# Performance work log

Measured on AMD Instinct MI355X. Metric: run time of the kernel, lower is better.

The kernel has to match this reference:

```python
import jax, jax.numpy as jnp
import numpy as np

N = 20000      # total nodes (1000 graphs x 20 nodes)
E = 160000     # total edges (avg degree 8)
B = 1000       # number of graphs
H = 2          # attention heads
C = 128        # out_channels per head (encoder_hidden)
D = H * C      # 256, node feature dim between layers
EMB = 64       # embed_dim / LSTM hidden
V = 5          # vocab
T = 21         # max_length decode steps
SOS = 1        # NT2IDX['U']
SQRT_C = float(np.sqrt(C))


def setup_inputs() -> dict:
    key = jax.random.key(0)
    ks = jax.random.split(key, 40)
    rn = lambda k, shape, s=0.05: (jax.random.normal(k, shape) * s).astype(jnp.float32)
    p = {}
    p['x'] = jax.random.normal(ks[0], (N, 4), jnp.float32)
    p['edge_index'] = jax.random.randint(ks[1], (2, E), 0, N)
    p['batch'] = jnp.repeat(jnp.arange(B), N // B)  # contiguous graph ids, all graphs nonempty
    p['gc_content'] = jax.random.uniform(ks[2], (B,), jnp.float32)
    p['seq_length'] = jnp.full((B,), 21.0, jnp.float32)
    # layer 0 TransformerConv (in=4 -> heads*C=256)
    p['c0_wq'] = rn(ks[3], (4, D)); p['c0_bq'] = rn(ks[4], (D,))
    p['c0_wk'] = rn(ks[5], (4, D)); p['c0_bk'] = rn(ks[6], (D,))
    p['c0_wv'] = rn(ks[7], (4, D)); p['c0_bv'] = rn(ks[8], (D,))
    p['c0_ws'] = rn(ks[9], (4, D)); p['c0_bs'] = rn(ks[10], (D,))
    # layers 1..2 stacked (in=256 -> 256)
    p['cw_q'] = rn(ks[11], (2, D, D)); p['cb_q'] = rn(ks[12], (2, D))
    p['cw_k'] = rn(ks[13], (2, D, D)); p['cb_k'] = rn(ks[14], (2, D))
    p['cw_v'] = rn(ks[15], (2, D, D)); p['cb_v'] = rn(ks[16], (2, D))
    p['cw_s'] = rn(ks[17], (2, D, D)); p['cb_s'] = rn(ks[18], (2, D))
    p['ln_g'] = jnp.ones((3, D), jnp.float32)
    p['ln_b'] = jnp.zeros((3, D), jnp.float32)
    p['enc_w'] = rn(ks[19], (D + 2, EMB)); p['enc_b'] = rn(ks[20], (EMB,))
    p['emb'] = rn(ks[21], (V, EMB), 1.0)
    p['w_ih'] = rn(ks[22], (EMB, 4 * EMB)); p['w_hh'] = rn(ks[23], (EMB, 4 * EMB))
    p['b_ih'] = rn(ks[24], (4 * EMB,)); p['b_hh'] = rn(ks[25], (4 * EMB,))
    p['fc_w'] = rn(ks[26], (EMB, V)); p['fc_b'] = rn(ks[27], (V,))
    return p


def _transformer_conv(x, src, tgt, wq, bq, wk, bk, wv, bv, ws, bs):
    # PyG TransformerConv, heads=H, concat=True, root_weight=True, no edge_attr.
    n = x.shape[0]
    q = (x @ wq + bq).reshape(n, H, C)[tgt]   # [E,H,C] query at target nodes
    k = (x @ wk + bk).reshape(n, H, C)[src]   # [E,H,C] key at source nodes
    v = (x @ wv + bv).reshape(n, H, C)[src]   # [E,H,C] value at source nodes
    score = (q * k).sum(-1) / SQRT_C          # [E,H]
    m = jax.ops.segment_max(score, tgt, num_segments=n)   # scatter-softmax (stable)
    a = jnp.exp(score - m[tgt])
    den = jax.ops.segment_sum(a, tgt, num_segments=n)
    alpha = a / den[tgt]                      # [E,H]
    out = jax.ops.segment_sum(alpha[..., None] * v, tgt, num_segments=n)  # [N,H,C]
    return out.reshape(n, D) + x @ ws + bs    # concat heads + skip (lin_skip)


def _layer_norm(x, g, b):
    mu = x.mean(-1, keepdims=True)
    var = ((x - mu) ** 2).mean(-1, keepdims=True)
    return (x - mu) * jax.lax.rsqrt(var + 1e-5) * g + b


def reference(x, edge_index, batch, gc_content, seq_length,
              c0_wq, c0_bq, c0_wk, c0_bk, c0_wv, c0_bv, c0_ws, c0_bs,
              cw_q, cb_q, cw_k, cb_k, cw_v, cb_v, cw_s, cb_s,
              ln_g, ln_b, enc_w, enc_b, emb, w_ih, w_hh, b_ih, b_hh, fc_w, fc_b):
    src, tgt = edge_index[0], edge_index[1]
    # ---- encoder: 3 TransformerConv + ReLU + LayerNorm (dropout=eval/identity) ----
    h = _transformer_conv(x, src, tgt, c0_wq, c0_bq, c0_wk, c0_bk, c0_wv, c0_bv, c0_ws, c0_bs)
    h = _layer_norm(jax.nn.relu(h), ln_g[0], ln_b[0])
    for i in range(2):
        h = _transformer_conv(h, src, tgt, cw_q[i], cb_q[i], cw_k[i], cb_k[i],
                              cw_v[i], cb_v[i], cw_s[i], cb_s[i])
        h = _layer_norm(jax.nn.relu(h), ln_g[i + 1], ln_b[i + 1])
    # ---- global mean pool per graph ----
    counts = jax.ops.segment_sum(jnp.ones((h.shape[0],), h.dtype), batch, num_segments=B)
    pool = jax.ops.segment_sum(h, batch, num_segments=B) / jnp.maximum(counts, 1.0)[:, None]
    gfeat = jnp.concatenate([pool, gc_content[:, None], seq_length[:, None]], axis=1)  # [B,258]
    enc = jax.nn.relu(gfeat @ enc_w + enc_b)  # [B,EMB]
    def step(carry, _):
        hs, cs, inp = carry
        g = inp @ w_ih + b_ih + hs @ w_hh + b_hh      # [B,4*EMB], torch gate order i,f,g,o
        i_g, f_g, g_g, o_g = jnp.split(g, 4, axis=-1)
        cs = jax.nn.sigmoid(f_g) * cs + jax.nn.sigmoid(i_g) * jnp.tanh(g_g)
        hs = jax.nn.sigmoid(o_g) * jnp.tanh(cs)
        logits = hs @ fc_w + fc_b                     # [B,V]
        tok = jnp.argmax(logits, axis=-1)
        return (hs, cs, emb[tok]), logits
    init = (enc, jnp.zeros_like(enc), jnp.broadcast_to(emb[SOS], (B, EMB)))
    _, logits = jax.lax.scan(step, init, None, length=T)  # [T,B,V]
    return jnp.transpose(logits, (1, 0, 2))               # [B,T,V]
```

## Files before the change

### kernel.cpp

```cpp
#include <hip/hip_runtime.h>
#include <math.h>

#define NN 20000
#define NNP 20096
#define NE 160000
#define NB 1000
#define EMB 64
#define NV 5
#define NT 21

typedef __attribute__((ext_vector_type(8))) short bf16x8;
typedef __attribute__((ext_vector_type(4))) float f32x4;

__device__ __forceinline__ float sigm(float x) { return 1.f / (1.f + expf(-x)); }

__device__ __forceinline__ ushort f2bf(float x) {
    unsigned u = __float_as_uint(x);
    unsigned r = (u + 0x7FFFu + ((u >> 16) & 1u)) >> 16;
    return (ushort)r;
}
__device__ __forceinline__ float bf2f(ushort h) {
    return __uint_as_float(((unsigned)h) << 16);
}

__device__ __forceinline__ void gl16(const ushort* g, ushort* l) {
    __builtin_amdgcn_global_load_lds((const __attribute__((address_space(1))) void*)g,
                                     (__attribute__((address_space(3))) void*)l, 16, 0, 0);
}

__global__ void k_fill(unsigned* p, int n, unsigned v) {
    int i = blockIdx.x * 256 + threadIdx.x;
    if (i < n) p[i] = v;
}

__global__ void k_count(const int* __restrict__ ei, int* __restrict__ deg,
                        int* __restrict__ bucket) {
    int e = blockIdx.x * 256 + threadIdx.x;
    if (e >= NE) return;
    int s = ei[e], t = ei[NE + e];
    int pos = atomicAdd(&deg[t], 1);
    if (pos < 64) bucket[(size_t)t * 64 + pos] = s;
}

__global__ void k_lin0(const float* __restrict__ x,
                       const float* __restrict__ wq, const float* __restrict__ bq,
                       const float* __restrict__ wk, const float* __restrict__ bk,
                       const float* __restrict__ wv, const float* __restrict__ bv,
                       const float* __restrict__ wss, const float* __restrict__ bss,
                       float* __restrict__ qkv, float* __restrict__ acc) {
    int idx = blockIdx.x * 256 + threadIdx.x;
    if (idx >= NN * 1024) return;
    int n = idx >> 10, j = idx & 1023;
    float x0 = x[n*4+0], x1 = x[n*4+1], x2 = x[n*4+2], x3 = x[n*4+3];
    const float* W; const float* bb; int col; float* outp;
    if (j < 256)      { W = wq;  bb = bq;  col = j;       outp = qkv + (size_t)n*768 + j; }
    else if (j < 512) { W = wk;  bb = bk;  col = j - 256; outp = qkv + (size_t)n*768 + j; }
    else if (j < 768) { W = wv;  bb = bv;  col = j - 512; outp = qkv + (size_t)n*768 + j; }
    else              { W = wss; bb = bss; col = j - 768; outp = acc + (size_t)n*256 + col; }
    float v = bb[col] + x0*W[col] + x1*W[256+col] + x2*W[512+col] + x3*W[768+col];
    *outp = v;
}

__global__ void k_convW(const float* __restrict__ cwq, const float* __restrict__ cwk,
                        const float* __restrict__ cwv, const float* __restrict__ cws,
                        ushort* __restrict__ WtHT, ushort* __restrict__ WtLT) {
    int idx = blockIdx.x * 256 + threadIdx.x;
    if (idx >= 2 * 64 * 1024) return;
    int n = idx & 1023;
    int rest = idx >> 10;
    int kq = rest & 63;
    int l = rest >> 6;
    int wsel = n >> 8, col = n & 255;
    const float* W = (wsel == 0) ? cwq : (wsel == 1) ? cwk : (wsel == 2) ? cwv : cws;
    W += (size_t)l * 65536;
    ushort hv[4], lv[4];
    #pragma unroll
    for (int i = 0; i < 4; ++i) {
        float v = W[(size_t)(kq * 4 + i) * 256 + col];
        hv[i] = f2bf(v);
        lv[i] = f2bf(v - bf2f(hv[i]));
    }
    int k0 = kq * 4;
    int kt = k0 >> 5, c = (k0 >> 3) & 3, j0 = k0 & 7;
    size_t o = ((size_t)l * 32 * 1024 + (size_t)(kt * 4 + c) * 1024 + n) * 8 + j0;
    *(ushort4*)(WtHT + o) = make_ushort4(hv[0], hv[1], hv[2], hv[3]);
    *(ushort4*)(WtLT + o) = make_ushort4(lv[0], lv[1], lv[2], lv[3]);
}

__global__ __launch_bounds__(256) void k_gemm4_mfma(
    const ushort* __restrict__ AhT, const ushort* __restrict__ AlT,
    const ushort* __restrict__ WtHT, const ushort* __restrict__ WtLT,
    const float* __restrict__ bq, const float* __restrict__ bk,
    const float* __restrict__ bv, const float* __restrict__ bs,
    float* __restrict__ qkv, float* __restrict__ acc) {
    __shared__ __align__(16) ushort SMEM[2][4][4][128][8];

    int id = blockIdx.x;
    int xcd = id & 7;
    int q8 = id >> 3;
    int s8 = q8 >> 3;
    int cblk = q8 & 7;
    int rblk = xcd + 8 * s8;
    if (rblk >= 157) return;
    int row0 = rblk * 128;
    int wsel = cblk >> 1;
    int coll = (cblk & 1) * 128;
    const float* bias; float* C; int ldc;
    if (wsel == 0)      { bias = bq; C = qkv;       ldc = 768; }
    else if (wsel == 1) { bias = bk; C = qkv + 256; ldc = 768; }
    else if (wsel == 2) { bias = bv; C = qkv + 512; ldc = 768; }
    else                { bias = bs; C = acc;       ldc = 256; }
    int ncol0 = cblk * 128;

    int tid = threadIdx.x;
    int w = tid >> 6, lane = tid & 63;
    int wr = w >> 1, wc = w & 1;
    int g = lane >> 4, r16 = lane & 15;

    const ushort* srcp; int rbase, rstr;
    if (w == 0)      { srcp = AhT;  rbase = row0;  rstr = NNP; }
    else if (w == 1) { srcp = AlT;  rbase = row0;  rstr = NNP; }
    else if (w == 2) { srcp = WtHT; rbase = ncol0; rstr = 1024; }
    else             { srcp = WtLT; rbase = ncol0; rstr = 1024; }
    ushort* lb0 = &SMEM[0][w][0][0][0];
    ushort* lb1 = &SMEM[1][w][0][0][0];

    const ushort* ap[8];
    #pragma unroll
    for (int i = 0; i < 8; ++i)
        ap[i] = srcp + ((size_t)((i >> 1) * rstr + rbase + (i & 1) * 64 + lane)) * 8;
    const size_t kstep = (size_t)4 * rstr * 8;

    f32x4 accv[4][4];
    f32x4 zz = {0.f, 0.f, 0.f, 0.f};
    #pragma unroll
    for (int m = 0; m < 4; ++m)
        #pragma unroll
        for (int n = 0; n < 4; ++n) accv[m][n] = zz;

    auto stage = [&](ushort* lb) {
        #pragma unroll
        for (int i = 0; i < 8; ++i) {
            gl16(ap[i], lb + i * 512);
            ap[i] += kstep;
        }
    };

    stage(lb0);
    for (int kt = 0; kt < 8; ++kt) {
        int cur = kt & 1;
        if (kt < 7) {
            stage(cur ? lb0 : lb1);
            asm volatile("s_waitcnt vmcnt(8)" ::: "memory");
        } else {
            asm volatile("s_waitcnt vmcnt(0)" ::: "memory");
        }
        __builtin_amdgcn_sched_barrier(0);
        __builtin_amdgcn_s_barrier();

        bf16x8 bH[4], bL[4];
        #pragma unroll
        for (int n = 0; n < 4; ++n) {
            int rw = wc * 64 + n * 16 + r16;
            bH[n] = *(const bf16x8*)&SMEM[cur][2][g][rw][0];
            bL[n] = *(const bf16x8*)&SMEM[cur][3][g][rw][0];
        }
        #pragma unroll
        for (int m = 0; m < 4; ++m) {
            int rw = wr * 64 + m * 16 + r16;
            bf16x8 aH = *(const bf16x8*)&SMEM[cur][0][g][rw][0];
            bf16x8 aL = *(const bf16x8*)&SMEM[cur][1][g][rw][0];
            #pragma unroll
            for (int n = 0; n < 4; ++n) {
                accv[m][n] = __builtin_amdgcn_mfma_f32_16x16x32_bf16(aH, bH[n], accv[m][n], 0, 0, 0);
                accv[m][n] = __builtin_amdgcn_mfma_f32_16x16x32_bf16(aH, bL[n], accv[m][n], 0, 0, 0);
                accv[m][n] = __builtin_amdgcn_mfma_f32_16x16x32_bf16(aL, bH[n], accv[m][n], 0, 0, 0);
            }
        }
        __builtin_amdgcn_s_barrier();
    }

    float* sl = (float*)&SMEM[0][0][0][0][0] + w * 1088;
    int erow = lane >> 2;
    int ecb  = (lane & 3) * 16;
    #pragma unroll
    for (int m = 0; m < 4; ++m) {
        #pragma unroll
        for (int n = 0; n < 4; ++n) {
            int cl = coll + wc * 64 + n * 16 + r16;
            float bvv = bias[cl];
            #pragma unroll
            for (int r = 0; r < 4; ++r)
                sl[(g * 4 + r) * 68 + n * 16 + r16] = accv[m][n][r] + bvv;
        }
        int grow = row0 + wr * 64 + m * 16 + erow;
        if (grow < NN) {
            float4 v0 = *(float4*)&sl[erow * 68 + ecb + 0];
            float4 v1 = *(float4*)&sl[erow * 68 + ecb + 4];
            float4 v2 = *(float4*)&sl[erow * 68 + ecb + 8];
            float4 v3 = *(float4*)&sl[erow * 68 + ecb + 12];
            float* cp = C + (size_t)grow * ldc + coll + wc * 64 + ecb;
            ((float4*)cp)[0] = v0; ((float4*)cp)[1] = v1;
            ((float4*)cp)[2] = v2; ((float4*)cp)[3] = v3;
        }
    }
}

__global__ __launch_bounds__(256) void k_attn_ln(const float* __restrict__ qkv,
                                                 const int* __restrict__ deg,
                                                 const int* __restrict__ bucket,
                                                 const float* __restrict__ acc,
                                                 const float* __restrict__ lg,
                                                 const float* __restrict__ lb,
                                                 ushort* __restrict__ AhT,
                                                 ushort* __restrict__ AlT) {
    __shared__ float ssc[4][64];
    __shared__ int ssrc[4][64];
    __shared__ __align__(16) float srow[2][256];
    int ws = threadIdx.x >> 6, l = threadIdx.x & 63;
    int t = blockIdx.x * 2 + (ws >> 1);
    int h = ws & 1;
    int cnt = deg[t]; if (cnt > 64) cnt = 64;
    const int* bptr = bucket + (size_t)t * 64;
    int gq = l >> 4, pos = l & 15;
    const float* qp = qkv + (size_t)t * 768 + h * 128 + pos * 8;
    float4 qa = *(const float4*)qp, qb = *(const float4*)(qp + 4);

    float m = -INFINITY, den = 0.f, o0 = 0.f, o1 = 0.f;
    for (int c0 = 0; c0 < cnt; c0 += 64) {
        int clen = cnt - c0; if (clen > 64) clen = 64;
        if (l < clen) ssrc[ws][l] = bptr[c0 + l];
        for (int e = gq; e < clen; e += 4) {
            int s = ssrc[ws][e];
            const float* kp = qkv + (size_t)s * 768 + 256 + h * 128 + pos * 8;
            float4 ka = *(const float4*)kp, kb = *(const float4*)(kp + 4);
            float d = qa.x*ka.x + qa.y*ka.y + qa.z*ka.z + qa.w*ka.w
                    + qb.x*kb.x + qb.y*kb.y + qb.z*kb.z + qb.w*kb.w;
            d += __shfl_xor(d, 1); d += __shfl_xor(d, 2);
            d += __shfl_xor(d, 4); d += __shfl_xor(d, 8);
            if (pos == 0) ssc[ws][e] = d * 0.08838834764831845f;
        }
        float sv = (l < clen) ? ssc[ws][l] : -INFINITY;
        float M = sv;
        #pragma unroll
        for (int off = 32; off; off >>= 1) M = fmaxf(M, __shfl_xor(M, off));
        float wl = (l < clen) ? expf(sv - M) : 0.f;
        float D = wl;
        #pragma unroll
        for (int off = 32; off; off >>= 1) D += __shfl_xor(D, off);
        ssc[ws][l] = wl;
        float nm = fmaxf(m, M);
        float so = expf(m - nm), sn = expf(M - nm);
        den = den * so + D * sn;
        o0 *= so; o1 *= so;
        float co0 = 0.f, co1 = 0.f;
        int p = 0;
        for (; p + 4 <= clen; p += 4) {
            float a0 = ssc[ws][p],     a1 = ssc[ws][p + 1];
            float a2 = ssc[ws][p + 2], a3 = ssc[ws][p + 3];
            int s0 = ssrc[ws][p],     s1 = ssrc[ws][p + 1];
            int s2 = ssrc[ws][p + 2], s3 = ssrc[ws][p + 3];
            float2 v0 = *(const float2*)(qkv + (size_t)s0 * 768 + 512 + h * 128 + l * 2);
            float2 v1 = *(const float2*)(qkv + (size_t)s1 * 768 + 512 + h * 128 + l * 2);
            float2 v2 = *(const float2*)(qkv + (size_t)s2 * 768 + 512 + h * 128 + l * 2);
            float2 v3 = *(const float2*)(qkv + (size_t)s3 * 768 + 512 + h * 128 + l * 2);
            co0 += a0 * v0.x + a1 * v1.x + a2 * v2.x + a3 * v3.x;
            co1 += a0 * v0.y + a1 * v1.y + a2 * v2.y + a3 * v3.y;
        }
        for (; p < clen; ++p) {
            float a = ssc[ws][p];
            int s = ssrc[ws][p];
            float2 v = *(const float2*)(qkv + (size_t)s * 768 + 512 + h * 128 + l * 2);
            co0 += a * v.x; co1 += a * v.y;
        }
        o0 += co0 * sn; o1 += co1 * sn;
        m = nm;
    }
    float inv = (den > 0.f) ? 1.f / den : 0.f;
    float2 sk = *(const float2*)(acc + (size_t)t * 256 + h * 128 + l * 2);
    float v0 = fmaxf(sk.x + o0 * inv, 0.f);
    float v1 = fmaxf(sk.y + o1 * inv, 0.f);
    *(float2*)&srow[ws >> 1][h * 128 + l * 2] = make_float2(v0, v1);
    __syncthreads();
    if (ws < 2) {
        int tt = blockIdx.x * 2 + ws;
        float4 v = *(const float4*)&srow[ws][l * 4];
        float sum = v.x + v.y + v.z + v.w;
        #pragma unroll
        for (int o = 32; o; o >>= 1) sum += __shfl_xor(sum, o);
        float mu = sum * (1.f / 256.f);
        float d0 = v.x - mu, d1 = v.y - mu, d2 = v.z - mu, d3 = v.w - mu;
        float sq = d0*d0 + d1*d1 + d2*d2 + d3*d3;
        #pragma unroll
        for (int o = 32; o; o >>= 1) sq += __shfl_xor(sq, o);
        float rs = rsqrtf(sq * (1.f / 256.f) + 1e-5f);
        int d = l * 4;
        float4 gg = *(const float4*)(lg + d);
        float4 bb = *(const float4*)(lb + d);
        float e0 = d0 * rs * gg.x + bb.x;
        float e1 = d1 * rs * gg.y + bb.y;
        float e2 = d2 * rs * gg.z + bb.z;
        float e3 = d3 * rs * gg.w + bb.w;
        ushort4 hv, lv;
        hv.x = f2bf(e0); lv.x = f2bf(e0 - bf2f(hv.x));
        hv.y = f2bf(e1); lv.y = f2bf(e1 - bf2f(hv.y));
        hv.z = f2bf(e2); lv.z = f2bf(e2 - bf2f(hv.z));
        hv.w = f2bf(e3); lv.w = f2bf(e3 - bf2f(hv.w));
        size_t o = ((size_t)(l >> 1) * NNP + tt) * 8 + (l & 1) * 4;
        *(ushort4*)(AhT + o) = hv;
        *(ushort4*)(AlT + o) = lv;
    }
}

__global__ __launch_bounds__(64) void k_poolenc(const ushort* __restrict__ AhT,
                                                const ushort* __restrict__ AlT,
                                                const float* __restrict__ gc,
                                                const float* __restrict__ seq,
                                                const float* __restrict__ ew,
                                                const float* __restrict__ eb,
                                                float* __restrict__ hs) {
    int b = blockIdx.x, j = threadIdx.x;
    __shared__ __align__(16) float pool[256];
    int r = j >> 1, j0 = (j & 1) * 4;
    float4 s4 = make_float4(0.f, 0.f, 0.f, 0.f);
    for (int n = 0; n < 20; ++n) {
        size_t o = ((size_t)r * NNP + b * 20 + n) * 8 + j0;
        ushort4 hv = *(const ushort4*)(AhT + o);
        ushort4 lv = *(const ushort4*)(AlT + o);
        s4.x += bf2f(hv.x) + bf2f(lv.x);
        s4.y += bf2f(hv.y) + bf2f(lv.y);
        s4.z += bf2f(hv.z) + bf2f(lv.z);
        s4.w += bf2f(hv.w) + bf2f(lv.w);
    }
    const float inv20 = 1.f / 20.f;
    s4.x *= inv20; s4.y *= inv20; s4.z *= inv20; s4.w *= inv20;
    *(float4*)(&pool[j * 4]) = s4;
    __syncthreads();
    float sacc = eb[j];
    for (int k = 0; k < 256; ++k) sacc += pool[k] * ew[k * 64 + j];
    sacc += gc[b] * ew[256 * 64 + j] + seq[b] * ew[257 * 64 + j];
    hs[(size_t)b * 64 + j] = fmaxf(sacc, 0.f);
}

__global__ void k_xc(const float* __restrict__ emb, const float* __restrict__ wih,
                     float* __restrict__ xc) {
    int idx = blockIdx.x * 256 + threadIdx.x;
    if (idx >= 5 * 256) return;
    int v = idx >> 8, col = idx & 255;
    float s = 0.f;
    for (int k = 0; k < 64; ++k) s += emb[v * 64 + k] * wih[k * 256 + col];
    xc[idx] = s;
}

__global__ __launch_bounds__(64, 1) void k_decode(const float* __restrict__ whh,
                                                  const float* __restrict__ bih,
                                                  const float* __restrict__ bhh,
                                                  const float* __restrict__ xc,
                                                  const float* __restrict__ fcw,
                                                  const float* __restrict__ fcb,
                                                  const float* __restrict__ hs0,
                                                  float* __restrict__ out) {
    int b = blockIdx.x;
    int j = threadIdx.x;

    float wgt[4][64];
    #pragma unroll
    for (int k = 0; k < 64; ++k) {
        #pragma unroll
        for (int g = 0; g < 4; ++g)
            wgt[g][k] = whh[k * 256 + g * 64 + j];
    }
    float bs0 = bih[0 * 64 + j] + bhh[0 * 64 + j];
    float bs1 = bih[1 * 64 + j] + bhh[1 * 64 + j];
    float bs2 = bih[2 * 64 + j] + bhh[2 * 64 + j];
    float bs3 = bih[3 * 64 + j] + bhh[3 * 64 + j];
    float xcg[5][4];
    #pragma unroll
    for (int v = 0; v < 5; ++v)
        #pragma unroll
        for (int g = 0; g < 4; ++g) xcg[v][g] = xc[v * 256 + g * 64 + j];
    float fw0 = fcw[j * 5 + 0], fw1 = fcw[j * 5 + 1], fw2 = fcw[j * 5 + 2],
          fw3 = fcw[j * 5 + 3], fw4 = fcw[j * 5 + 4];
    float fb0 = fcb[0], fb1 = fcb[1], fb2 = fcb[2], fb3 = fcb[3], fb4 = fcb[4];

    float hj = hs0[(size_t)b * 64 + j];
    float cj = 0.f;
    int tok = 1;

    for (int t = 0; t < NT; ++t) {
        float xg0, xg1, xg2, xg3;
        if (tok == 0)      { xg0 = xcg[0][0]; xg1 = xcg[0][1]; xg2 = xcg[0][2]; xg3 = xcg[0][3]; }
        else if (tok == 1) { xg0 = xcg[1][0]; xg1 = xcg[1][1]; xg2 = xcg[1][2]; xg3 = xcg[1][3]; }
        else if (tok == 2) { xg0 = xcg[2][0]; xg1 = xcg[2][1]; xg2 = xcg[2][2]; xg3 = xcg[2][3]; }
        else if (tok == 3) { xg0 = xcg[3][0]; xg1 = xcg[3][1]; xg2 = xcg[3][2]; xg3 = xcg[3][3]; }
        else               { xg0 = xcg[4][0]; xg1 = xcg[4][1]; xg2 = xcg[4][2]; xg3 = xcg[4][3]; }
        float aA0 = 0.f, aA1 = 0.f, aA2 = 0.f, aA3 = 0.f;
        float aB0 = 0.f, aB1 = 0.f, aB2 = 0.f, aB3 = 0.f;
        #pragma unroll
        for (int k = 0; k < 64; k += 2) {
            float h0 = __uint_as_float(__builtin_amdgcn_readlane(__float_as_uint(hj), k));
            float h1 = __uint_as_float(__builtin_amdgcn_readlane(__float_as_uint(hj), k + 1));
            aA0 += h0 * wgt[0][k]; aA1 += h0 * wgt[1][k];
            aA2 += h0 * wgt[2][k]; aA3 += h0 * wgt[3][k];
            aB0 += h1 * wgt[0][k + 1]; aB1 += h1 * wgt[1][k + 1];
            aB2 += h1 * wgt[2][k + 1]; aB3 += h1 * wgt[3][k + 1];
        }
        float ig = sigm(bs0 + xg0 + (aA0 + aB0));
        float fg = sigm(bs1 + xg1 + (aA1 + aB1));
        float gt = tanhf(bs2 + xg2 + (aA2 + aB2));
        float og = sigm(bs3 + xg3 + (aA3 + aB3));
        cj = fg * cj + ig * gt;
        hj = og * tanhf(cj);
        float l0 = hj * fw0, l1 = hj * fw1, l2 = hj * fw2, l3 = hj * fw3, l4 = hj * fw4;
        #pragma unroll
        for (int off = 32; off; off >>= 1) {
            l0 += __shfl_xor(l0, off); l1 += __shfl_xor(l1, off);
            l2 += __shfl_xor(l2, off); l3 += __shfl_xor(l3, off);
            l4 += __shfl_xor(l4, off);
        }
        l0 += fb0; l1 += fb1; l2 += fb2; l3 += fb3; l4 += fb4;
        int tk = 0; float bv = l0;
        if (l1 > bv) { bv = l1; tk = 1; }
        if (l2 > bv) { bv = l2; tk = 2; }
        if (l3 > bv) { bv = l3; tk = 3; }
        if (l4 > bv) { bv = l4; tk = 4; }
        tok = tk;
        if (j < 5) {
            float myl = (j == 0) ? l0 : (j == 1) ? l1 : (j == 2) ? l2 : (j == 3) ? l3 : l4;
            out[(size_t)b * (NT * NV) + t * NV + j] = myl;
        }
    }
}

extern "C" void kernel_launch(void* const* d_in, const int* in_sizes, int n_in,
                              void* d_out, int out_size, void* d_ws, size_t ws_size,
                              hipStream_t stream) {
    const float* x    = (const float*)d_in[0];
    const int*   ei   = (const int*)d_in[1];
    const float* gc   = (const float*)d_in[3];
    const float* seq  = (const float*)d_in[4];
    const float* c0wq = (const float*)d_in[5];  const float* c0bq = (const float*)d_in[6];
    const float* c0wk = (const float*)d_in[7];  const float* c0bk = (const float*)d_in[8];
    const float* c0wv = (const float*)d_in[9];  const float* c0bv = (const float*)d_in[10];
    const float* c0ws = (const float*)d_in[11]; const float* c0bs = (const float*)d_in[12];
    const float* cwq  = (const float*)d_in[13]; const float* cbq  = (const float*)d_in[14];
    const float* cwk  = (const float*)d_in[15]; const float* cbk  = (const float*)d_in[16];
    const float* cwv  = (const float*)d_in[17]; const float* cbv  = (const float*)d_in[18];
    const float* cws  = (const float*)d_in[19]; const float* cbs  = (const float*)d_in[20];
    const float* lng  = (const float*)d_in[21]; const float* lnb  = (const float*)d_in[22];
    const float* ew   = (const float*)d_in[23]; const float* eb   = (const float*)d_in[24];
    const float* emb  = (const float*)d_in[25];
    const float* wih  = (const float*)d_in[26]; const float* whh  = (const float*)d_in[27];
    const float* bih  = (const float*)d_in[28]; const float* bhh  = (const float*)d_in[29];
    const float* fcw  = (const float*)d_in[30]; const float* fcb  = (const float*)d_in[31];
    (void)in_sizes; (void)n_in; (void)out_size; (void)ws_size;

    float* wsf  = (float*)d_ws;
    float* qkv  = wsf;
    float* acc  = qkv + (size_t)NN * 768;
    ushort* AhT = (ushort*)(acc + (size_t)NN * 256);
    ushort* AlT = AhT + (size_t)32 * NNP * 8;
    ushort* WtHT = AlT + (size_t)32 * NNP * 8;
    ushort* WtLT = WtHT + 2 * 32 * 1024 * 8;
    float* xc   = (float*)(WtLT + 2 * 32 * 1024 * 8);
    float* hs   = xc + 5 * 256;
    int* deg    = (int*)(hs + (size_t)NB * 64);
    int* bucket = deg + NN;

    k_fill<<<(NN + 255) / 256, 256, 0, stream>>>((unsigned*)deg, NN, 0u);
    k_count<<<(NE + 255) / 256, 256, 0, stream>>>(ei, deg, bucket);
    k_convW<<<512, 256, 0, stream>>>(cwq, cwk, cwv, cws, WtHT, WtLT);
    k_xc<<<5, 256, 0, stream>>>(emb, wih, xc);

    for (int L = 0; L < 3; ++L) {
        if (L == 0) {
            k_lin0<<<NN * 1024 / 256, 256, 0, stream>>>(x, c0wq, c0bq, c0wk, c0bk,
                                                        c0wv, c0bv, c0ws, c0bs, qkv, acc);
        } else {
            int i = L - 1;
            k_gemm4_mfma<<<1280, 256, 0, stream>>>(AhT, AlT,
                WtHT + (size_t)i * 32 * 1024 * 8, WtLT + (size_t)i * 32 * 1024 * 8,
                cbq + i * 256, cbk + i * 256, cbv + i * 256, cbs + i * 256,
                qkv, acc);
        }
        k_attn_ln<<<NN / 2, 256, 0, stream>>>(qkv, deg, bucket, acc,
                                              lng + L * 256, lnb + L * 256, AhT, AlT);
    }
    k_poolenc<<<NB, 64, 0, stream>>>(AhT, AlT, gc, seq, ew, eb, hs);
    k_decode<<<NB, 64, 0, stream>>>(whh, bih, bhh, xc, fcw, fcb, hs, (float*)d_out);
}
```

Measured before the change: 383.8 us.

## Load GEMM A operand directly into registers and halve LDS staging

The MFMA GEMM now reads the A (activation hi/lo) fragments straight from global memory into registers each k-step. Only the B (weight hi/lo) tiles are still double-buffered through LDS, so LDS drops from 64KB to 32KB per block. Launch bounds now request 3 blocks per SM so more waves can hide latency. The cost is duplicated A loads across the two column warps and more register pressure, and waits on A loads now depend on the compiler's vmcnt tracking.

New measurement: 377.1 us. Within noise of the previous version (-1.7%).

```diff
diff --git a/kernel.cpp b/kernel.cpp
--- a/kernel.cpp
+++ b/kernel.cpp
@@ -87,13 +87,13 @@
     *(ushort4*)(WtLT + o) = make_ushort4(lv[0], lv[1], lv[2], lv[3]);
 }
 
-__global__ __launch_bounds__(256) void k_gemm4_mfma(
+__global__ __launch_bounds__(256, 3) void k_gemm4_mfma(
     const ushort* __restrict__ AhT, const ushort* __restrict__ AlT,
     const ushort* __restrict__ WtHT, const ushort* __restrict__ WtLT,
     const float* __restrict__ bq, const float* __restrict__ bk,
     const float* __restrict__ bv, const float* __restrict__ bs,
     float* __restrict__ qkv, float* __restrict__ acc) {
-    __shared__ __align__(16) ushort SMEM[2][4][4][128][8];
+    __shared__ __align__(16) ushort SB[2][2][4][128][8];
 
     int id = blockIdx.x;
     int xcd = id & 7;
@@ -117,19 +117,20 @@
     int wr = w >> 1, wc = w & 1;
     int g = lane >> 4, r16 = lane & 15;
 
-    const ushort* srcp; int rbase, rstr;
-    if (w == 0)      { srcp = AhT;  rbase = row0;  rstr = NNP; }
-    else if (w == 1) { srcp = AlT;  rbase = row0;  rstr = NNP; }
-    else if (w == 2) { srcp = WtHT; rbase = ncol0; rstr = 1024; }
-    else             { srcp = WtLT; rbase = ncol0; rstr = 1024; }
-    ushort* lb0 = &SMEM[0][w][0][0][0];
-    ushort* lb1 = &SMEM[1][w][0][0][0];
-
-    const ushort* ap[8];
-    #pragma unroll
-    for (int i = 0; i < 8; ++i)
-        ap[i] = srcp + ((size_t)((i >> 1) * rstr + rbase + (i & 1) * 64 + lane)) * 8;
-    const size_t kstep = (size_t)4 * rstr * 8;
+    int hl = w >> 1;
+    const ushort* bsrc0 = (hl == 0) ? WtHT : WtLT;
+    const ushort* bS[4];
+    #pragma unroll
+    for (int i = 0; i < 4; ++i) {
+        int c = (w & 1) * 2 + (i >> 1);
+        int half = i & 1;
+        bS[i] = bsrc0 + ((size_t)c * 1024 + ncol0 + half * 64 + lane) * 8;
+    }
+    const size_t bstep = (size_t)4 * 1024 * 8;
+
+    const ushort* aPH = AhT + ((size_t)g * NNP + row0 + wr * 64 + r16) * 8;
+    const ushort* aPL = AlT + ((size_t)g * NNP + row0 + wr * 64 + r16) * 8;
+    const size_t astep = (size_t)4 * NNP * 8;
 
     f32x4 accv[4][4];
     f32x4 zz = {0.f, 0.f, 0.f, 0.f};
@@ -138,22 +139,31 @@
         #pragma unroll
         for (int n = 0; n < 4; ++n) accv[m][n] = zz;
 
-    auto stage = [&](ushort* lb) {
-        #pragma unroll
-        for (int i = 0; i < 8; ++i) {
-            gl16(ap[i], lb + i * 512);
-            ap[i] += kstep;
+    auto stageB = [&](int buf) {
+        #pragma unroll
+        for (int i = 0; i < 4; ++i) {
+            int c = (w & 1) * 2 + (i >> 1);
+            int half = i & 1;
+            gl16(bS[i], &SB[buf][hl][c][half * 64][0]);
+            bS[i] += bstep;
         }
     };
 
-    stage(lb0);
+    stageB(0);
     for (int kt = 0; kt < 8; ++kt) {
         int cur = kt & 1;
+        bf16x8 aH[4], aL[4];
+        #pragma unroll
+        for (int m = 0; m < 4; ++m) {
+            aH[m] = *(const bf16x8*)(aPH + m * 128);
+            aL[m] = *(const bf16x8*)(aPL + m * 128);
+        }
+        aPH += astep; aPL += astep;
         if (kt < 7) {
-            stage(cur ? lb0 : lb1);
+            stageB(cur ^ 1);
+            asm volatile("s_waitcnt vmcnt(12)" ::: "memory");
+        } else {
             asm volatile("s_waitcnt vmcnt(8)" ::: "memory");
-        } else {
-            asm volatile("s_waitcnt vmcnt(0)" ::: "memory");
         }
         __builtin_amdgcn_sched_barrier(0);
         __builtin_amdgcn_s_barrier();
@@ -162,25 +172,22 @@
         #pragma unroll
         for (int n = 0; n < 4; ++n) {
             int rw = wc * 64 + n * 16 + r16;
-            bH[n] = *(const bf16x8*)&SMEM[cur][2][g][rw][0];
-            bL[n] = *(const bf16x8*)&SMEM[cur][3][g][rw][0];
+            bH[n] = *(const bf16x8*)&SB[cur][0][g][rw][0];
+            bL[n] = *(const bf16x8*)&SB[cur][1][g][rw][0];
         }
         #pragma unroll
         for (int m = 0; m < 4; ++m) {
-            int rw = wr * 64 + m * 16 + r16;
-            bf16x8 aH = *(const bf16x8*)&SMEM[cur][0][g][rw][0];
-            bf16x8 aL = *(const bf16x8*)&SMEM[cur][1][g][rw][0];
             #pragma unroll
             for (int n = 0; n < 4; ++n) {
-                accv[m][n] = __builtin_amdgcn_mfma_f32_16x16x32_bf16(aH, bH[n], accv[m][n], 0, 0, 0);
-                accv[m][n] = __builtin_amdgcn_mfma_f32_16x16x32_bf16(aH, bL[n], accv[m][n], 0, 0, 0);
-                accv[m][n] = __builtin_amdgcn_mfma_f32_16x16x32_bf16(aL, bH[n], accv[m][n], 0, 0, 0);
+                accv[m][n] = __builtin_amdgcn_mfma_f32_16x16x32_bf16(aH[m], bH[n], accv[m][n], 0, 0, 0);
+                accv[m][n] = __builtin_amdgcn_mfma_f32_16x16x32_bf16(aH[m], bL[n], accv[m][n], 0, 0, 0);
+                accv[m][n] = __builtin_amdgcn_mfma_f32_16x16x32_bf16(aL[m], bH[n], accv[m][n], 0, 0, 0);
             }
         }
         __builtin_amdgcn_s_barrier();
     }
 
-    float* sl = (float*)&SMEM[0][0][0][0][0] + w * 1088;
+    float* sl = (float*)&SB[0][0][0][0][0] + w * 1088;
     int erow = lane >> 2;
     int ecb  = (lane & 3) * 16;
     #pragma unroll
```
